# Optimization experiments

Hardware: AMD Instinct MI355X
Metric: run time of the kernel (lower is better)

The kernel has to match this reference:

```python
import jax, jax.numpy as jnp
import numpy as np

WINDOW_SIZE = 11
B, C, H, W = 32, 1, 512, 512

def _create_window(ws: int) -> jnp.ndarray:
    x = np.arange(ws)
    gauss = np.exp(-((x - ws // 2) ** 2) / 2.0)
    gauss = gauss / gauss.sum()
    win = gauss[None, :] * gauss[:, None]  # [ws, ws]
    return jnp.asarray(win[None, None], dtype=jnp.float32)  # [1,1,ws,ws]

def setup_inputs() -> dict:
    key = jax.random.key(0)
    k1, k2 = jax.random.split(key)
    pred = jax.random.uniform(k1, (B, C, H, W), dtype=jnp.float32)
    target = jax.random.uniform(k2, (B, C, H, W), dtype=jnp.float32)
    window = _create_window(WINDOW_SIZE)
    return {"pred": pred, "target": target, "window": window}

def _conv(x, window):
    # SAME padding == padding=ws//2 for odd ws, stride 1
    return jax.lax.conv_general_dilated(
        x, window, window_strides=(1, 1), padding="SAME",
        dimension_numbers=("NCHW", "OIHW", "NCHW"))

def reference(pred, target, window):
    mu1 = _conv(pred, window)
    mu2 = _conv(target, window)
    mu1_sq = mu1 * mu1
    mu2_sq = mu2 * mu2
    mu1_mu2 = mu1 * mu2
    sigma1_sq = _conv(pred * pred, window) - mu1_sq
    sigma2_sq = _conv(target * target, window) - mu2_sq
    sigma12 = _conv(pred * target, window) - mu1_mu2
    C1 = 0.01 ** 2
    C2 = 0.03 ** 2
    ssim_map = ((2.0 * mu1_mu2 + C1) * (2.0 * sigma12 + C2)) / (
        (mu1_sq + mu2_sq + C1) * (sigma1_sq + sigma2_sq + C2))
    return 1.0 - jnp.mean(ssim_map)
```

## Files before the change

kernel.cpp:

```cpp
#include <hip/hip_runtime.h>

#define NB 32
#define HH 512
#define WW 512
#define WS 11
#define RAD 5
#define TX 256
#define YB 16
#define NR (YB + 2*RAD)
#define XCHUNKS (WW / TX)
#define YSTRIPS (HH / YB)
#define NBLK (NB * XCHUNKS * YSTRIPS)

__global__ __launch_bounds__(256, 4)
void ssim_main(const float* __restrict__ pred,
               const float* __restrict__ targ,
               const float* __restrict__ win,
               float* __restrict__ partial)
{
    __shared__ float2 rowbuf[2][TX + 2*RAD];

    const int tid = threadIdx.x;
    const int bid = blockIdx.x;
    const int chunk  = bid & (XCHUNKS - 1);
    const int t2     = bid >> 1;
    const int ystrip = t2 & (YSTRIPS - 1);
    const int img    = t2 >> 5;

    const int x0 = chunk * TX;
    const int y0 = ystrip * YB;
    const int x  = x0 + tid;

    const float g[WS] = {
        1.4867195e-06f, 1.3383023e-04f, 4.4318484e-03f, 5.3990967e-02f,
        2.4197073e-01f, 3.9894228e-01f, 2.4197073e-01f, 5.3990967e-02f,
        4.4318484e-03f, 1.3383023e-04f, 1.4867195e-06f };

    const float* __restrict__ pimg = pred + (size_t)img * (HH*WW);
    const float* __restrict__ timg = targ + (size_t)img * (HH*WW);

    float rp[WS], rt[WS], rss[WS], rpt[WS];

    float pm, tm, ph, th;
    float npm, ntm, nph, nth;

    auto fetch = [&](int r, float& a, float& b, float& c, float& d) {
        const int yin = y0 - RAD + r;
        a = 0.f; b = 0.f; c = 0.f; d = 0.f;
        if (yin >= 0 && yin < HH) {
            const float* prow = pimg + yin * WW;
            const float* trow = timg + yin * WW;
            a = prow[x];
            b = trow[x];
            if (tid < 2*RAD) {
                const int l = (tid < RAD) ? tid : (tid + TX);
                const int col = x0 - RAD + l;
                if (col >= 0 && col < WW) { c = prow[col]; d = trow[col]; }
            }
        }
    };

    fetch(0, pm, tm, ph, th);

    float acc = 0.f;
    const float C1 = 1.0e-4f, C2 = 9.0e-4f;

    #pragma unroll 1
    for (int rb = 0; rb < (NR + WS - 1) / WS; ++rb) {
        #pragma unroll
        for (int j = 0; j < WS; ++j) {
            const int r = rb * WS + j;
            if (r < NR) {
                const int par = r & 1;
                rowbuf[par][tid + RAD] = make_float2(pm, tm);
                if (tid < 2*RAD) {
                    const int l = (tid < RAD) ? tid : (tid + TX);
                    rowbuf[par][l] = make_float2(ph, th);
                }
                if (r + 1 < NR) fetch(r + 1, npm, ntm, nph, nth);
                __syncthreads();

                {
                    float sp = 0.f, st = 0.f, sss = 0.f, spt = 0.f;
                    #pragma unroll
                    for (int k = 0; k < WS; ++k) {
                        const float2 v = rowbuf[par][tid + k];
                        const float gk = g[k];
                        const float gp = gk * v.x;
                        const float gt = gk * v.y;
                        sp += gp;
                        st += gt;
                        sss = fmaf(gp, v.x, sss);
                        sss = fmaf(gt, v.y, sss);
                        spt = fmaf(gp, v.y, spt);
                    }
                    rp[j] = sp; rt[j] = st; rss[j] = sss; rpt[j] = spt;
                }

                if (r >= 2*RAD) {
                    float mu1 = 0.f, mu2 = 0.f, css = 0.f, cpt = 0.f;
                    #pragma unroll
                    for (int k = 0; k < WS; ++k) {
                        const int s = (j + 1 + k) % WS;
                        const float gk = g[k];
                        mu1 = fmaf(gk, rp[s],  mu1);
                        mu2 = fmaf(gk, rt[s],  mu2);
                        css = fmaf(gk, rss[s], css);
                        cpt = fmaf(gk, rpt[s], cpt);
                    }
                    const float m11 = mu1 * mu1;
                    const float m22 = mu2 * mu2;
                    const float m12 = mu1 * mu2;
                    const float msum = m11 + m22;
                    const float num = (2.f*m12 + C1) * (2.f*(cpt - m12) + C2);
                    const float den = (msum + C1) * ((css - msum) + C2);
                    acc += __fdividef(num, den);
                }
                pm = npm; tm = ntm; ph = nph; th = nth;
            }
        }
    }

    #pragma unroll
    for (int off = 32; off > 0; off >>= 1)
        acc += __shfl_down(acc, off, 64);
    __shared__ float red[4];
    if ((tid & 63) == 0) red[tid >> 6] = acc;
    __syncthreads();
    if (tid == 0) partial[bid] = red[0] + red[1] + red[2] + red[3];
}

__global__ void ssim_final(const float* __restrict__ partial, float* __restrict__ out)
{
    const int tid = threadIdx.x;
    float v = 0.f;
    #pragma unroll
    for (int i = 0; i < NBLK / 256; ++i)
        v += partial[tid + 256 * i];
    #pragma unroll
    for (int off = 32; off > 0; off >>= 1)
        v += __shfl_down(v, off, 64);
    __shared__ float red[4];
    if ((tid & 63) == 0) red[tid >> 6] = v;
    __syncthreads();
    if (tid == 0)
        out[0] = 1.f - (red[0] + red[1] + red[2] + red[3]) / (float)(NB * HH * WW);
}

extern "C" void kernel_launch(void* const* d_in, const int* in_sizes, int n_in,
                              void* d_out, int out_size, void* d_ws, size_t ws_size,
                              hipStream_t stream) {
    const float* pred = (const float*)d_in[0];
    const float* targ = (const float*)d_in[1];
    const float* win  = (const float*)d_in[2];
    float* out = (float*)d_out;
    float* partial = (float*)d_ws;

    ssim_main<<<NBLK, TX, 0, stream>>>(pred, targ, win, partial);
    ssim_final<<<1, 256, 0, stream>>>(partial, out);
}
```

Measured before the change: 136.5 us.

## Widen blocks to full image rows and stage per-pixel products in LDS planes

Each block now spans the full 512-pixel row width instead of two 256-wide chunks. This removes the per-row x-halo global loads and their bounds checks; the zero border columns are written once at kernel start. The LDS row buffer is split into four scalar planes (p, t, p*t, p²+t²), so the products are formed once per pixel and the horizontal 11-tap pass becomes four plain FMAs per tap. The trade-off is roughly twice the LDS read volume per row, four scalar reads per tap instead of one float2, plus 512-thread blocks with a larger barrier scope.

```diff
diff --git a/kernel.cpp b/kernel.cpp
--- a/kernel.cpp
+++ b/kernel.cpp
@@ -5,62 +5,53 @@
 #define WW 512
 #define WS 11
 #define RAD 5
-#define TX 256
+#define TX2 512
 #define YB 16
 #define NR (YB + 2*RAD)
-#define XCHUNKS (WW / TX)
 #define YSTRIPS (HH / YB)
-#define NBLK (NB * XCHUNKS * YSTRIPS)
+#define NBLK (NB * YSTRIPS)
+#define LDSW (TX2 + 2*RAD + 6)
 
-__global__ __launch_bounds__(256, 4)
+__global__ __launch_bounds__(TX2, 4)
 void ssim_main(const float* __restrict__ pred,
                const float* __restrict__ targ,
                const float* __restrict__ win,
                float* __restrict__ partial)
 {
-    __shared__ float2 rowbuf[2][TX + 2*RAD];
+    __shared__ float lds[2][4][LDSW];
 
     const int tid = threadIdx.x;
     const int bid = blockIdx.x;
-    const int chunk  = bid & (XCHUNKS - 1);
-    const int t2     = bid >> 1;
-    const int ystrip = t2 & (YSTRIPS - 1);
-    const int img    = t2 >> 5;
-
-    const int x0 = chunk * TX;
+    const int ystrip = bid & (YSTRIPS - 1);
+    const int img    = bid >> 5;
     const int y0 = ystrip * YB;
-    const int x  = x0 + tid;
 
     const float g[WS] = {
         1.4867195e-06f, 1.3383023e-04f, 4.4318484e-03f, 5.3990967e-02f,
         2.4197073e-01f, 3.9894228e-01f, 2.4197073e-01f, 5.3990967e-02f,
         4.4318484e-03f, 1.3383023e-04f, 1.4867195e-06f };
 
-    const float* __restrict__ pimg = pred + (size_t)img * (HH*WW);
-    const float* __restrict__ timg = targ + (size_t)img * (HH*WW);
+    if (tid < 2*RAD) {
+        const int c = (tid < RAD) ? tid : (tid - RAD + TX2 + RAD);
+        #pragma unroll
+        for (int pa = 0; pa < 2; ++pa)
+            #pragma unroll
+            for (int f = 0; f < 4; ++f)
+                lds[pa][f][c] = 0.f;
+    }
+
+    const float* pcur = pred + (size_t)img * (HH*WW) + (ptrdiff_t)(y0 - RAD) * WW + tid;
+    const float* tcur = targ + (size_t)img * (HH*WW) + (ptrdiff_t)(y0 - RAD) * WW + tid;
 
     float rp[WS], rt[WS], rss[WS], rpt[WS];
 
-    float pm, tm, ph, th;
-    float npm, ntm, nph, nth;
+    float pm, tm, npm, ntm;
 
-    auto fetch = [&](int r, float& a, float& b, float& c, float& d) {
-        const int yin = y0 - RAD + r;
-        a = 0.f; b = 0.f; c = 0.f; d = 0.f;
-        if (yin >= 0 && yin < HH) {
-            const float* prow = pimg + yin * WW;
-            const float* trow = timg + yin * WW;
-            a = prow[x];
-            b = trow[x];
-            if (tid < 2*RAD) {
-                const int l = (tid < RAD) ? tid : (tid + TX);
-                const int col = x0 - RAD + l;
-                if (col >= 0 && col < WW) { c = prow[col]; d = trow[col]; }
-            }
-        }
-    };
-
-    fetch(0, pm, tm, ph, th);
+    {
+        const int yin = y0 - RAD;
+        if (yin >= 0) { pm = pcur[0]; tm = tcur[0]; } else { pm = 0.f; tm = 0.f; }
+        pcur += WW; tcur += WW;
+    }
 
     float acc = 0.f;
     const float C1 = 1.0e-4f, C2 = 9.0e-4f;
@@ -72,29 +63,30 @@
             const int r = rb * WS + j;
             if (r < NR) {
                 const int par = r & 1;
-                rowbuf[par][tid + RAD] = make_float2(pm, tm);
-                if (tid < 2*RAD) {
-                    const int l = (tid < RAD) ? tid : (tid + TX);
-                    rowbuf[par][l] = make_float2(ph, th);
+                lds[par][0][tid + RAD] = pm;
+                lds[par][1][tid + RAD] = tm;
+                lds[par][2][tid + RAD] = pm * tm;
+                lds[par][3][tid + RAD] = fmaf(pm, pm, tm * tm);
+
+                if (r + 1 < NR) {
+                    const int yin = y0 - RAD + r + 1;
+                    if (yin >= 0 && yin < HH) { npm = pcur[0]; ntm = tcur[0]; }
+                    else                      { npm = 0.f;     ntm = 0.f; }
+                    pcur += WW; tcur += WW;
                 }
-                if (r + 1 < NR) fetch(r + 1, npm, ntm, nph, nth);
                 __syncthreads();
 
                 {
-                    float sp = 0.f, st = 0.f, sss = 0.f, spt = 0.f;
+                    float sp = 0.f, st = 0.f, spt = 0.f, sss = 0.f;
                     #pragma unroll
                     for (int k = 0; k < WS; ++k) {
-                        const float2 v = rowbuf[par][tid + k];
                         const float gk = g[k];
-                        const float gp = gk * v.x;
-                        const float gt = gk * v.y;
-                        sp += gp;
-                        st += gt;
-                        sss = fmaf(gp, v.x, sss);
-                        sss = fmaf(gt, v.y, sss);
-                        spt = fmaf(gp, v.y, spt);
+                        sp  = fmaf(gk, lds[par][0][tid + k], sp);
+                        st  = fmaf(gk, lds[par][1][tid + k], st);
+                        spt = fmaf(gk, lds[par][2][tid + k], spt);
+                        sss = fmaf(gk, lds[par][3][tid + k], sss);
                     }
-                    rp[j] = sp; rt[j] = st; rss[j] = sss; rpt[j] = spt;
+                    rp[j] = sp; rt[j] = st; rpt[j] = spt; rss[j] = sss;
                 }
 
                 if (r >= 2*RAD) {
@@ -116,7 +108,7 @@
                     const float den = (msum + C1) * ((css - msum) + C2);
                     acc += __fdividef(num, den);
                 }
-                pm = npm; tm = ntm; ph = nph; th = nth;
+                pm = npm; tm = ntm;
             }
         }
     }
@@ -124,10 +116,15 @@
     #pragma unroll
     for (int off = 32; off > 0; off >>= 1)
         acc += __shfl_down(acc, off, 64);
-    __shared__ float red[4];
+    __shared__ float red[8];
     if ((tid & 63) == 0) red[tid >> 6] = acc;
     __syncthreads();
-    if (tid == 0) partial[bid] = red[0] + red[1] + red[2] + red[3];
+    if (tid == 0) {
+        float s = 0.f;
+        #pragma unroll
+        for (int w = 0; w < 8; ++w) s += red[w];
+        partial[bid] = s;
+    }
 }
 
 __global__ void ssim_final(const float* __restrict__ partial, float* __restrict__ out)
@@ -156,6 +153,6 @@
     float* out = (float*)d_out;
     float* partial = (float*)d_ws;
 
-    ssim_main<<<NBLK, TX, 0, stream>>>(pred, targ, win, partial);
+    ssim_main<<<NBLK, TX2, 0, stream>>>(pred, targ, win, partial);
     ssim_final<<<1, 256, 0, stream>>>(partial, out);
 }
```

Result: slower. 140.0 us (+2.6%).
